# Kernel tuning notes

Measured on AMD Instinct MI355X. Metric: run time of the kernel, lower is better.

Reference implementation:

```python
import jax, jax.numpy as jnp
import numpy as np

B, S, E, D = 8, 2048, 1024, 64

def setup_inputs() -> dict:
    key = jax.random.key(0)
    k1, k2, k3, k4 = jax.random.split(key, 4)
    x = jax.random.normal(k1, (B, S, E), dtype=jnp.float32)
    attention_mask = jnp.ones((B, S, S), dtype=jnp.int32)
    scale = 1.0 / np.sqrt(E)
    Wq = jax.random.normal(k2, (E, D), dtype=jnp.float32) * scale
    Wk = jax.random.normal(k3, (E, D), dtype=jnp.float32) * scale
    Wv = jax.random.normal(k4, (E, D), dtype=jnp.float32) * scale
    return {"x": x, "attention_mask": attention_mask, "Wq": Wq, "Wk": Wk, "Wv": Wv}

def reference(x, attention_mask, Wq, Wk, Wv):
    # Q,K,V projections: [B,S,E] @ [E,D] -> [B,S,D]
    Q = jnp.einsum('bse,ed->bsd', x, Wq)
    K = jnp.einsum('bse,ed->bsd', x, Wk)
    V = jnp.einsum('bse,ed->bsd', x, Wv)
    d_head = Q.shape[-1]
    # scores: [B,S,S], scaled by sqrt(dim_head)
    scores = jnp.einsum('bqd,bkd->bqk', Q, K) / jnp.sqrt(jnp.asarray(d_head, Q.dtype))
    scores = jnp.where(attention_mask == 0, jnp.asarray(-jnp.inf, scores.dtype), scores)
    attn = jax.nn.softmax(scores, axis=-1)
    # dropout p=0.0 (eval mode) -> identity
    out = jnp.einsum('bqk,bkd->bqd', attn, V)
    return out
```

## Files before the change

kernel.cpp:

```cpp
#include <hip/hip_runtime.h>
#include <hip/hip_bf16.h>
#include <math.h>


typedef __attribute__((ext_vector_type(8))) short short8;
typedef __attribute__((ext_vector_type(4))) float v4f;

__device__ __forceinline__ unsigned short f2bf(float f) {
  unsigned int u = __float_as_uint(f);
  unsigned int r = (u + 0x7fffu + ((u >> 16) & 1u)) >> 16;
  return (unsigned short)r;
}

__device__ __forceinline__ void gl_lds16(const void* g, void* l) {
  __builtin_amdgcn_global_load_lds(
      (__attribute__((address_space(1))) unsigned int*)(g),
      (__attribute__((address_space(3))) unsigned int*)(l), 16, 0, 0);
}

__global__ __launch_bounds__(256) void prep_wf(const float* __restrict__ Wq,
                                               const float* __restrict__ Wk,
                                               const float* __restrict__ Wv,
                                               unsigned short* __restrict__ Wf) {
  int o = blockIdx.x * 256 + threadIdx.x;
  int j = o & 7;
  int lane = (o >> 3) & 63;
  int c = o >> 9;
  int kk = c & 1;
  int nt = (c % 24) >> 1;
  int kt = c / 24;
  int q = lane & 15, quad = lane >> 4;
  int n = nt * 16 + q;
  int k = kt * 64 + kk * 32 + quad * 8 + j;
  const float* W = (n < 64) ? Wq : (n < 128 ? Wk : Wv);
  Wf[o] = f2bf(W[(size_t)k * 64 + (n & 63)]);
}

__global__ __launch_bounds__(512) void proj_kernel(const float* __restrict__ x,
                                                   const unsigned short* __restrict__ Wf,
                                                   unsigned short* __restrict__ Qg,
                                                   unsigned short* __restrict__ Kf,
                                                   unsigned short* __restrict__ Vf) {
  __shared__ __align__(16) unsigned short wl[2][24 * 512];

  const int tid = threadIdx.x;
  const int w = tid >> 6;
  const int lane = tid & 63;
  const int q = lane & 15, quad = lane >> 4;
  const int m0 = blockIdx.x * 64;
  const int mrow = (w & 3) * 16;
  const int noff = (w >> 2) * 6;

  const float* xrow = x + (size_t)(m0 + mrow + q) * 1024 + quad * 8;

  v4f acc[6];
#pragma unroll
  for (int i = 0; i < 6; i++) acc[i] = (v4f)(0.0f);

  auto stageB = [&](int kt, int buf) {
    for (int t = w; t < 24; t += 8)
      gl_lds16(Wf + ((size_t)kt * 24 + t) * 512 + lane * 8, &wl[buf][t * 512]);
  };

  float4 acur[4], anext[4];
  auto loadA = [&](int kt, float4 a[4]) {
    const float* p = xrow + kt * 64;
    a[0] = *reinterpret_cast<const float4*>(p);
    a[1] = *reinterpret_cast<const float4*>(p + 4);
    a[2] = *reinterpret_cast<const float4*>(p + 32);
    a[3] = *reinterpret_cast<const float4*>(p + 36);
  };

  stageB(0, 0);
  loadA(0, acur);

  for (int kt = 0; kt < 16; kt++) {
    __syncthreads();
    if (kt < 15) {
      stageB(kt + 1, (kt + 1) & 1);
      loadA(kt + 1, anext);
    }
    short8 af0, af1;
    {
      float* f = reinterpret_cast<float*>(acur);
#pragma unroll
      for (int j = 0; j < 4; j++) { af0[j] = (short)f2bf(f[j]); af0[4 + j] = (short)f2bf(f[4 + j]); }
#pragma unroll
      for (int j = 0; j < 4; j++) { af1[j] = (short)f2bf(f[8 + j]); af1[4 + j] = (short)f2bf(f[12 + j]); }
    }
    const unsigned short* bufp = &wl[kt & 1][0];
#pragma unroll
    for (int i = 0; i < 6; i++) {
      int t = noff + i;
      short8 b0 = *reinterpret_cast<const short8*>(&bufp[(t * 2 + 0) * 512 + lane * 8]);
      short8 b1 = *reinterpret_cast<const short8*>(&bufp[(t * 2 + 1) * 512 + lane * 8]);
      acc[i] = __builtin_amdgcn_mfma_f32_16x16x32_bf16(af0, b0, acc[i], 0, 0, 0);
      acc[i] = __builtin_amdgcn_mfma_f32_16x16x32_bf16(af1, b1, acc[i], 0, 0, 0);
    }
#pragma unroll
    for (int i = 0; i < 4; i++) acur[i] = anext[i];
  }

#pragma unroll
  for (int i = 0; i < 6; i++) {
    const int n = (noff + i) * 16 + q;
#pragma unroll
    for (int r = 0; r < 4; r++) {
      const int m = m0 + mrow + quad * 4 + r;
      const unsigned short hv = f2bf(acc[i][r]);
      if (n < 64) {
        Qg[(size_t)m * 64 + n] = hv;
      } else if (n < 128) {
        const int d = n - 64, s = m;
        const int b = s >> 11, srem = s & 2047, g = srem >> 4, qi = srem & 15;
        const int kk2 = d >> 5, quad2 = (d >> 3) & 3, j2 = d & 7;
        Kf[((((size_t)b * 128 + g) * 2 + kk2) * 64 + quad2 * 16 + qi) * 8 + j2] = hv;
      } else {
        const int d = n - 128, s = m;
        const int b = s >> 11, srem = s & 2047, kt2 = srem >> 6, s6 = srem & 63;
        const int kk2 = s6 >> 5, quad2 = (s6 >> 3) & 3, j2 = s6 & 7;
        const int dt = d >> 4, qi = d & 15;
        Vf[(((((size_t)b * 32 + kt2) * 4 + dt) * 2 + kk2) * 64 + quad2 * 16 + qi) * 8 + j2] = hv;
      }
    }
  }
}

__global__ __launch_bounds__(512) void attn_kernel(const unsigned short* __restrict__ Qg,
                                                   const unsigned short* __restrict__ Kf,
                                                   const unsigned short* __restrict__ Vf,
                                                   const int* __restrict__ maskg,
                                                   float* __restrict__ outg) {
  __shared__ __align__(16) unsigned short KV[2][2][16 * 512];
  __shared__ __align__(16) unsigned short Pl[8][16][72];

  const int tid = threadIdx.x;
  const int qt = blockIdx.x, b = blockIdx.y;
  const int q0 = qt * 64;
  const int w = tid >> 6, lane = tid & 63;
  const int g = w >> 2, wq = w & 3;
  const int q = lane & 15, quad = lane >> 4;
  const int myrow = wq * 16 + quad * 4;

  const size_t qbase = ((size_t)b * 2048 + q0 + wq * 16 + q) * 64 + quad * 8;
  const short8 qf0 = *reinterpret_cast<const short8*>(&Qg[qbase]);
  const short8 qf1 = *reinterpret_cast<const short8*>(&Qg[qbase + 32]);

  short8 onesf;
#pragma unroll
  for (int j = 0; j < 8; j++) onesf[j] = (short)0x3F80;

  auto stage = [&](int kt, int buf) {
#pragma unroll
    for (int i = 0; i < 4; i++) {
      const int t = wq * 4 + i;
      const unsigned short* src =
          (t < 8)
              ? Kf + (((size_t)b * 128 + kt * 4 + (t >> 1)) * 2 + (t & 1)) * 512
              : Vf + ((((size_t)b * 32 + kt) * 4 + ((t - 8) >> 1)) * 2 + (t & 1)) * 512;
      gl_lds16(src + lane * 8, &KV[g][buf][t * 512]);
    }
  };

  const int* mp = maskg + ((size_t)b * 2048 + q0 + myrow) * 2048 + q;
  int mcur[16], mnext[16];
  auto loadmask = [&](int kt, int* m) {
#pragma unroll
    for (int r = 0; r < 4; r++)
#pragma unroll
      for (int nt = 0; nt < 4; nt++)
        m[r * 4 + nt] = mp[(size_t)r * 2048 + kt * 64 + nt * 16];
  };

  v4f o_acc[4], l_acc;
#pragma unroll
  for (int dt = 0; dt < 4; dt++) o_acc[dt] = (v4f)(0.0f);
  l_acc = (v4f)(0.0f);

  const float SC = 0.125f * 1.4426950408889634f;

  stage(g * 16, 0);
  loadmask(g * 16, mcur);

  for (int it = 0; it < 16; it++) {
    const int kt = g * 16 + it;
    __syncthreads();
    if (it < 15) {
      stage(kt + 1, (it + 1) & 1);
      loadmask(kt + 1, mnext);
    }
    const unsigned short* bufp = &KV[g][it & 1][0];

    v4f s_acc[4];
#pragma unroll
    for (int nt = 0; nt < 4; nt++) s_acc[nt] = (v4f)(0.0f);
#pragma unroll
    for (int nt = 0; nt < 4; nt++) {
      short8 b0 = *reinterpret_cast<const short8*>(&bufp[(nt * 2 + 0) * 512 + lane * 8]);
      short8 b1 = *reinterpret_cast<const short8*>(&bufp[(nt * 2 + 1) * 512 + lane * 8]);
      s_acc[nt] = __builtin_amdgcn_mfma_f32_16x16x32_bf16(qf0, b0, s_acc[nt], 0, 0, 0);
      s_acc[nt] = __builtin_amdgcn_mfma_f32_16x16x32_bf16(qf1, b1, s_acc[nt], 0, 0, 0);
    }

#pragma unroll
    for (int nt = 0; nt < 4; nt++)
#pragma unroll
      for (int r = 0; r < 4; r++) {
        float bias = (mcur[r * 4 + nt] == 0) ? -INFINITY : 0.0f;
        float p = exp2f(fmaf(s_acc[nt][r], SC, bias));
        Pl[w][quad * 4 + r][nt * 16 + q] = f2bf(p);
      }

    short8 pf0 = *reinterpret_cast<const short8*>(&Pl[w][q][quad * 8]);
    short8 pf1 = *reinterpret_cast<const short8*>(&Pl[w][q][32 + quad * 8]);

#pragma unroll
    for (int dt = 0; dt < 4; dt++) {
      short8 v0 = *reinterpret_cast<const short8*>(&bufp[(8 + dt * 2 + 0) * 512 + lane * 8]);
      short8 v1 = *reinterpret_cast<const short8*>(&bufp[(8 + dt * 2 + 1) * 512 + lane * 8]);
      o_acc[dt] = __builtin_amdgcn_mfma_f32_16x16x32_bf16(pf0, v0, o_acc[dt], 0, 0, 0);
      o_acc[dt] = __builtin_amdgcn_mfma_f32_16x16x32_bf16(pf1, v1, o_acc[dt], 0, 0, 0);
    }
    l_acc = __builtin_amdgcn_mfma_f32_16x16x32_bf16(pf0, onesf, l_acc, 0, 0, 0);
    l_acc = __builtin_amdgcn_mfma_f32_16x16x32_bf16(pf1, onesf, l_acc, 0, 0, 0);

#pragma unroll
    for (int i = 0; i < 16; i++) mcur[i] = mnext[i];
  }

  __syncthreads();
  float* Of = (float*)&KV[0][0][0];
  float* Lf = (float*)&Pl[0][0][0];
  if (g == 1) {
#pragma unroll
    for (int r = 0; r < 4; r++) {
      const int row = myrow + r;
#pragma unroll
      for (int dt = 0; dt < 4; dt++) Of[row * 65 + dt * 16 + q] = o_acc[dt][r];
      if (q == 0) Lf[row] = l_acc[r];
    }
  }
  __syncthreads();
  if (g == 0) {
#pragma unroll
    for (int r = 0; r < 4; r++) {
      const int row = myrow + r;
      const float inv = 1.0f / (l_acc[r] + Lf[row]);
      const size_t orow = ((size_t)b * 2048 + q0 + row) * 64;
#pragma unroll
      for (int dt = 0; dt < 4; dt++)
        outg[orow + dt * 16 + q] = (o_acc[dt][r] + Of[row * 65 + dt * 16 + q]) * inv;
    }
  }
}

extern "C" void kernel_launch(void* const* d_in, const int* in_sizes, int n_in,
                              void* d_out, int out_size, void* d_ws, size_t ws_size,
                              hipStream_t stream) {
  const float* x = (const float*)d_in[0];
  const int* mask = (const int*)d_in[1];
  const float* Wq = (const float*)d_in[2];
  const float* Wk = (const float*)d_in[3];
  const float* Wv = (const float*)d_in[4];
  float* out = (float*)d_out;

  char* ws = (char*)d_ws;
  unsigned short* Qg = (unsigned short*)(ws);
  unsigned short* Kf = (unsigned short*)(ws + (size_t)(2 << 20));
  unsigned short* Vf = (unsigned short*)(ws + (size_t)(4 << 20));
  unsigned short* Wf = (unsigned short*)(ws + (size_t)(6 << 20));

  prep_wf<<<768, 256, 0, stream>>>(Wq, Wk, Wv, Wf);
  proj_kernel<<<256, 512, 0, stream>>>(x, Wf, Qg, Kf, Vf);
  attn_kernel<<<dim3(32, 8), 512, 0, stream>>>(Qg, Kf, Vf, mask, out);
}
```

Baseline: 278.3 us.

## Drop LDS staging, split attention keys across four waves, and use mask bitmask

Result: slower. 301.2 us (+8.2%).

```diff
diff --git a/kernel.cpp b/kernel.cpp
--- a/kernel.cpp
+++ b/kernel.cpp
@@ -10,12 +10,6 @@
   unsigned int u = __float_as_uint(f);
   unsigned int r = (u + 0x7fffu + ((u >> 16) & 1u)) >> 16;
   return (unsigned short)r;
-}
-
-__device__ __forceinline__ void gl_lds16(const void* g, void* l) {
-  __builtin_amdgcn_global_load_lds(
-      (__attribute__((address_space(1))) unsigned int*)(g),
-      (__attribute__((address_space(3))) unsigned int*)(l), 16, 0, 0);
 }
 
 __global__ __launch_bounds__(256) void prep_wf(const float* __restrict__ Wq,
@@ -41,26 +35,19 @@
                                                    unsigned short* __restrict__ Qg,
                                                    unsigned short* __restrict__ Kf,
                                                    unsigned short* __restrict__ Vf) {
-  __shared__ __align__(16) unsigned short wl[2][24 * 512];
-
   const int tid = threadIdx.x;
   const int w = tid >> 6;
   const int lane = tid & 63;
   const int q = lane & 15, quad = lane >> 4;
-  const int m0 = blockIdx.x * 64;
-  const int mrow = (w & 3) * 16;
-  const int noff = (w >> 2) * 6;
-
-  const float* xrow = x + (size_t)(m0 + mrow + q) * 1024 + quad * 8;
-
-  v4f acc[6];
-#pragma unroll
-  for (int i = 0; i < 6; i++) acc[i] = (v4f)(0.0f);
-
-  auto stageB = [&](int kt, int buf) {
-    for (int t = w; t < 24; t += 8)
-      gl_lds16(Wf + ((size_t)kt * 24 + t) * 512 + lane * 8, &wl[buf][t * 512]);
-  };
+  const int rg = w >> 2, ng = w & 3;
+  const int m0 = blockIdx.x * 32 + rg * 16;
+
+  const float* xrow = x + (size_t)(m0 + q) * 1024 + quad * 8;
+  const unsigned short* Wl = Wf + lane * 8;
+
+  v4f acc[3];
+#pragma unroll
+  for (int i = 0; i < 3; i++) acc[i] = (v4f)(0.0f);
 
   float4 acur[4], anext[4];
   auto loadA = [&](int kt, float4 a[4]) {
@@ -71,15 +58,10 @@
     a[3] = *reinterpret_cast<const float4*>(p + 36);
   };
 
-  stageB(0, 0);
   loadA(0, acur);
 
   for (int kt = 0; kt < 16; kt++) {
-    __syncthreads();
-    if (kt < 15) {
-      stageB(kt + 1, (kt + 1) & 1);
-      loadA(kt + 1, anext);
-    }
+    if (kt < 15) loadA(kt + 1, anext);
     short8 af0, af1;
     {
       float* f = reinterpret_cast<float*>(acur);
@@ -88,25 +70,26 @@
 #pragma unroll
       for (int j = 0; j < 4; j++) { af1[j] = (short)f2bf(f[8 + j]); af1[4 + j] = (short)f2bf(f[12 + j]); }
     }
-    const unsigned short* bufp = &wl[kt & 1][0];
-#pragma unroll
-    for (int i = 0; i < 6; i++) {
-      int t = noff + i;
-      short8 b0 = *reinterpret_cast<const short8*>(&bufp[(t * 2 + 0) * 512 + lane * 8]);
-      short8 b1 = *reinterpret_cast<const short8*>(&bufp[(t * 2 + 1) * 512 + lane * 8]);
+    __builtin_amdgcn_s_setprio(1);
+#pragma unroll
+    for (int i = 0; i < 3; i++) {
+      const size_t toff = ((size_t)kt * 24 + (ng * 3 + i) * 2) * 512;
+      short8 b0 = *reinterpret_cast<const short8*>(Wl + toff);
+      short8 b1 = *reinterpret_cast<const short8*>(Wl + toff + 512);
       acc[i] = __builtin_amdgcn_mfma_f32_16x16x32_bf16(af0, b0, acc[i], 0, 0, 0);
       acc[i] = __builtin_amdgcn_mfma_f32_16x16x32_bf16(af1, b1, acc[i], 0, 0, 0);
     }
+    __builtin_amdgcn_s_setprio(0);
 #pragma unroll
     for (int i = 0; i < 4; i++) acur[i] = anext[i];
   }
 
 #pragma unroll
-  for (int i = 0; i < 6; i++) {
-    const int n = (noff + i) * 16 + q;
-#pragma unroll
-    for (int r = 0; r < 4; r++) {
-      const int m = m0 + mrow + quad * 4 + r;
+  for (int i = 0; i < 3; i++) {
+    const int n = (ng * 3 + i) * 16 + q;
+#pragma unroll
+    for (int r = 0; r < 4; r++) {
+      const int m = m0 + quad * 4 + r;
       const unsigned short hv = f2bf(acc[i][r]);
       if (n < 64) {
         Qg[(size_t)m * 64 + n] = hv;
@@ -126,23 +109,21 @@
   }
 }
 
-__global__ __launch_bounds__(512) void attn_kernel(const unsigned short* __restrict__ Qg,
-                                                   const unsigned short* __restrict__ Kf,
-                                                   const unsigned short* __restrict__ Vf,
-                                                   const int* __restrict__ maskg,
-                                                   float* __restrict__ outg) {
-  __shared__ __align__(16) unsigned short KV[2][2][16 * 512];
-  __shared__ __align__(16) unsigned short Pl[8][16][72];
+__global__ __launch_bounds__(256, 3) void attn_kernel(const unsigned short* __restrict__ Qg,
+                                                      const unsigned short* __restrict__ Kf,
+                                                      const unsigned short* __restrict__ Vf,
+                                                      const int* __restrict__ maskg,
+                                                      float* __restrict__ outg) {
+  __shared__ __align__(16) unsigned short Pl[4][16][72];
 
   const int tid = threadIdx.x;
-  const int qt = blockIdx.x, b = blockIdx.y;
-  const int q0 = qt * 64;
+  const int bid = blockIdx.x;
+  const int b = bid & 7, qt = bid >> 3;
+  const int q0 = qt * 16;
   const int w = tid >> 6, lane = tid & 63;
-  const int g = w >> 2, wq = w & 3;
   const int q = lane & 15, quad = lane >> 4;
-  const int myrow = wq * 16 + quad * 4;
-
-  const size_t qbase = ((size_t)b * 2048 + q0 + wq * 16 + q) * 64 + quad * 8;
+
+  const size_t qbase = ((size_t)b * 2048 + q0 + q) * 64 + quad * 8;
   const short8 qf0 = *reinterpret_cast<const short8*>(&Qg[qbase]);
   const short8 qf1 = *reinterpret_cast<const short8*>(&Qg[qbase + 32]);
 
@@ -150,27 +131,9 @@
 #pragma unroll
   for (int j = 0; j < 8; j++) onesf[j] = (short)0x3F80;
 
-  auto stage = [&](int kt, int buf) {
-#pragma unroll
-    for (int i = 0; i < 4; i++) {
-      const int t = wq * 4 + i;
-      const unsigned short* src =
-          (t < 8)
-              ? Kf + (((size_t)b * 128 + kt * 4 + (t >> 1)) * 2 + (t & 1)) * 512
-              : Vf + ((((size_t)b * 32 + kt) * 4 + ((t - 8) >> 1)) * 2 + (t & 1)) * 512;
-      gl_lds16(src + lane * 8, &KV[g][buf][t * 512]);
-    }
-  };
-
-  const int* mp = maskg + ((size_t)b * 2048 + q0 + myrow) * 2048 + q;
-  int mcur[16], mnext[16];
-  auto loadmask = [&](int kt, int* m) {
-#pragma unroll
-    for (int r = 0; r < 4; r++)
-#pragma unroll
-      for (int nt = 0; nt < 4; nt++)
-        m[r * 4 + nt] = mp[(size_t)r * 2048 + kt * 64 + nt * 16];
-  };
+  const unsigned short* Kb = Kf + (size_t)b * 131072 + lane * 8;
+  const unsigned short* Vb = Vf + (size_t)b * 131072 + lane * 8;
+  const int* mb = maskg + ((size_t)b * 2048 + q0 + quad) * 2048 + q * 4;
 
   v4f o_acc[4], l_acc;
 #pragma unroll
@@ -178,78 +141,124 @@
   l_acc = (v4f)(0.0f);
 
   const float SC = 0.125f * 1.4426950408889634f;
-
-  stage(g * 16, 0);
-  loadmask(g * 16, mcur);
-
-  for (int it = 0; it < 16; it++) {
-    const int kt = g * 16 + it;
-    __syncthreads();
-    if (it < 15) {
-      stage(kt + 1, (it + 1) & 1);
-      loadmask(kt + 1, mnext);
-    }
-    const unsigned short* bufp = &KV[g][it & 1][0];
+  const int kt0 = w * 8;
+
+  unsigned zb = 0;
+  {
+    int4 m4[4];
+#pragma unroll
+    for (int j = 0; j < 4; j++)
+      m4[j] = *reinterpret_cast<const int4*>(mb + (size_t)j * 8192 + kt0 * 64);
+#pragma unroll
+    for (int j = 0; j < 4; j++)
+      zb |= ((unsigned)(m4[j].x == 0) << (j * 4)) | ((unsigned)(m4[j].y == 0) << (j * 4 + 1)) |
+            ((unsigned)(m4[j].z == 0) << (j * 4 + 2)) | ((unsigned)(m4[j].w == 0) << (j * 4 + 3));
+  }
+
+#pragma unroll
+  for (int it = 0; it < 8; it++) {
+    const int kt = kt0 + it;
+
+    int4 m4[4];
+    if (it < 7) {
+#pragma unroll
+      for (int j = 0; j < 4; j++)
+        m4[j] = *reinterpret_cast<const int4*>(mb + (size_t)j * 8192 + (kt + 1) * 64);
+    }
 
     v4f s_acc[4];
-#pragma unroll
-    for (int nt = 0; nt < 4; nt++) s_acc[nt] = (v4f)(0.0f);
+    __builtin_amdgcn_s_setprio(1);
 #pragma unroll
     for (int nt = 0; nt < 4; nt++) {
-      short8 b0 = *reinterpret_cast<const short8*>(&bufp[(nt * 2 + 0) * 512 + lane * 8]);
-      short8 b1 = *reinterpret_cast<const short8*>(&bufp[(nt * 2 + 1) * 512 + lane * 8]);
-      s_acc[nt] = __builtin_amdgcn_mfma_f32_16x16x32_bf16(qf0, b0, s_acc[nt], 0, 0, 0);
-      s_acc[nt] = __builtin_amdgcn_mfma_f32_16x16x32_bf16(qf1, b1, s_acc[nt], 0, 0, 0);
-    }
+      short8 k0 = *reinterpret_cast<const short8*>(Kb + ((size_t)kt * 8 + nt * 2 + 0) * 512);
+      short8 k1 = *reinterpret_cast<const short8*>(Kb + ((size_t)kt * 8 + nt * 2 + 1) * 512);
+      s_acc[nt] = __builtin_amdgcn_mfma_f32_16x16x32_bf16(qf0, k0, (v4f)(0.0f), 0, 0, 0);
+      s_acc[nt] = __builtin_amdgcn_mfma_f32_16x16x32_bf16(qf1, k1, s_acc[nt], 0, 0, 0);
+    }
+    __builtin_amdgcn_s_setprio(0);
 
 #pragma unroll
     for (int nt = 0; nt < 4; nt++)
 #pragma unroll
-      for (int r = 0; r < 4; r++) {
-        float bias = (mcur[r * 4 + nt] == 0) ? -INFINITY : 0.0f;
-        float p = exp2f(fmaf(s_acc[nt][r], SC, bias));
-        Pl[w][quad * 4 + r][nt * 16 + q] = f2bf(p);
-      }
-
-    short8 pf0 = *reinterpret_cast<const short8*>(&Pl[w][q][quad * 8]);
-    short8 pf1 = *reinterpret_cast<const short8*>(&Pl[w][q][32 + quad * 8]);
-
+      for (int r = 0; r < 4; r++)
+        Pl[w][quad * 4 + r][nt * 16 + q] = f2bf(exp2f(s_acc[nt][r] * SC));
+
+    if (__any(zb != 0u)) {
+#pragma unroll
+      for (int j = 0; j < 4; j++)
+#pragma unroll
+        for (int c = 0; c < 4; c++)
+          if ((zb >> (j * 4 + c)) & 1u) Pl[w][j * 4 + quad][q * 4 + c] = 0;
+    }
+
+    const short8 pf0 = *reinterpret_cast<const short8*>(&Pl[w][q][quad * 8]);
+    const short8 pf1 = *reinterpret_cast<const short8*>(&Pl[w][q][32 + quad * 8]);
+
+    __builtin_amdgcn_s_setprio(1);
 #pragma unroll
     for (int dt = 0; dt < 4; dt++) {
-      short8 v0 = *reinterpret_cast<const short8*>(&bufp[(8 + dt * 2 + 0) * 512 + lane * 8]);
-      short8 v1 = *reinterpret_cast<const short8*>(&bufp[(8 + dt * 2 + 1) * 512 + lane * 8]);
+      short8 v0 = *reinterpret_cast<const short8*>(Vb + ((size_t)kt * 8 + dt * 2 + 0) * 512);
+      short8 v1 = *reinterpret_cast<const short8*>(Vb + ((size_t)kt * 8 + dt * 2 + 1) * 512);
       o_acc[dt] = __builtin_amdgcn_mfma_f32_16x16x32_bf16(pf0, v0, o_acc[dt], 0, 0, 0);
       o_acc[dt] = __builtin_amdgcn_mfma_f32_16x16x32_bf16(pf1, v1, o_acc[dt], 0, 0, 0);
     }
     l_acc = __builtin_amdgcn_mfma_f32_16x16x32_bf16(pf0, onesf, l_acc, 0, 0, 0);
     l_acc = __builtin_amdgcn_mfma_f32_16x16x32_bf16(pf1, onesf, l_acc, 0, 0, 0);
-
-#pragma unroll
-    for (int i = 0; i < 16; i++) mcur[i] = mnext[i];
-  }
-
-  __syncthreads();
-  float* Of = (float*)&KV[0][0][0];
-  float* Lf = (float*)&Pl[0][0][0];
-  if (g == 1) {
-#pragma unroll
-    for (int r = 0; r < 4; r++) {
-      const int row = myrow + r;
-#pragma unroll
-      for (int dt = 0; dt < 4; dt++) Of[row * 65 + dt * 16 + q] = o_acc[dt][r];
-      if (q == 0) Lf[row] = l_acc[r];
-    }
-  }
-  __syncthreads();
-  if (g == 0) {
-#pragma unroll
-    for (int r = 0; r < 4; r++) {
-      const int row = myrow + r;
-      const float inv = 1.0f / (l_acc[r] + Lf[row]);
+    __builtin_amdgcn_s_setprio(0);
+
+    if (it < 7) {
+      zb = 0;
+#pragma unroll
+      for (int j = 0; j < 4; j++)
+        zb |= ((unsigned)(m4[j].x == 0) << (j * 4)) | ((unsigned)(m4[j].y == 0) << (j * 4 + 1)) |
+              ((unsigned)(m4[j].z == 0) << (j * 4 + 2)) | ((unsigned)(m4[j].w == 0) << (j * 4 + 3));
+    }
+  }
+
+  __syncthreads();
+  float* Osf = reinterpret_cast<float*>(&Pl[0][0][0]);
+  float* Lsf = Osf + 2 * 16 * 68;
+
+  if (w >= 2) {
+    const int wi = w - 2;
+#pragma unroll
+    for (int r = 0; r < 4; r++) {
+      const int row = quad * 4 + r;
+#pragma unroll
+      for (int dt = 0; dt < 4; dt++) Osf[(wi * 16 + row) * 68 + dt * 16 + q] = o_acc[dt][r];
+      if (q == 0) Lsf[wi * 16 + row] = l_acc[r];
+    }
+  }
+  __syncthreads();
+  if (w < 2) {
+#pragma unroll
+    for (int r = 0; r < 4; r++) {
+      const int row = quad * 4 + r;
+#pragma unroll
+      for (int dt = 0; dt < 4; dt++) o_acc[dt][r] += Osf[(w * 16 + row) * 68 + dt * 16 + q];
+      l_acc[r] += Lsf[w * 16 + row];
+    }
+  }
+  __syncthreads();
+  if (w == 1) {
+#pragma unroll
+    for (int r = 0; r < 4; r++) {
+      const int row = quad * 4 + r;
+#pragma unroll
+      for (int dt = 0; dt < 4; dt++) Osf[row * 68 + dt * 16 + q] = o_acc[dt][r];
+      if (q == 0) Lsf[row] = l_acc[r];
+    }
+  }
+  __syncthreads();
+  if (w == 0) {
+#pragma unroll
+    for (int r = 0; r < 4; r++) {
+      const int row = quad * 4 + r;
+      const float inv = 1.0f / (l_acc[r] + Lsf[row]);
       const size_t orow = ((size_t)b * 2048 + q0 + row) * 64;
 #pragma unroll
       for (int dt = 0; dt < 4; dt++)
-        outg[orow + dt * 16 + q] = (o_acc[dt][r] + Of[row * 65 + dt * 16 + q]) * inv;
+        outg[orow + dt * 16 + q] = (o_acc[dt][r] + Osf[row * 68 + dt * 16 + q]) * inv;
     }
   }
 }
@@ -271,6 +280,6 @@
   unsigned short* Wf = (unsigned short*)(ws + (size_t)(6 << 20));
 
   prep_wf<<<768, 256, 0, stream>>>(Wq, Wk, Wv, Wf);
-  proj_kernel<<<256, 512, 0, stream>>>(x, Wf, Qg, Kf, Vf);
-  attn_kernel<<<dim3(32, 8), 512, 0, stream>>>(Qg, Kf, Vf, mask, out);
-}
+  proj_kernel<<<512, 512, 0, stream>>>(x, Wf, Qg, Kf, Vf);
+  attn_kernel<<<1024, 256, 0, stream>>>(Qg, Kf, Vf, mask, out);
+}
```
